# Performance work log

Hardware: AMD Instinct MI355X
Metric: run time of the kernel (lower is better)

Reference implementation:

```python
import jax, jax.numpy as jnp
import numpy as np

N_NODES = 50000
N_EDGES = 800000
IN_DIM = 96
HID = 96
OUT_DIM = 32
N_GRAPHS = 256


def setup_inputs() -> dict:
    key = jax.random.key(0)
    ks = jax.random.split(key, 12)
    x = jax.random.normal(ks[0], (N_NODES, IN_DIM), dtype=jnp.float32)
    edge_index = jax.random.randint(ks[1], (2, N_EDGES), 0, N_NODES, dtype=jnp.int64)
    batch = jnp.sort(jax.random.randint(ks[2], (N_NODES,), 0, N_GRAPHS, dtype=jnp.int64))
    s = 1.0 / np.sqrt(HID)
    W1 = jax.random.normal(ks[3], (IN_DIM, HID), dtype=jnp.float32) * s
    W2 = jax.random.normal(ks[4], (HID, HID), dtype=jnp.float32) * s
    W3 = jax.random.normal(ks[5], (HID, HID), dtype=jnp.float32) * s
    fc_w = jax.random.normal(ks[6], (HID, OUT_DIM), dtype=jnp.float32) * s
    return {
        'x': x, 'edge_index': edge_index, 'batch': batch,
        'W1': W1, 'b1': jnp.zeros((HID,), jnp.float32),
        'W2': W2, 'b2': jnp.zeros((HID,), jnp.float32),
        'W3': W3, 'b3': jnp.zeros((HID,), jnp.float32),
        'fc_w': fc_w, 'fc_b': jnp.zeros((OUT_DIM,), jnp.float32),
    }


def _gcn_conv(h, row, col, norm, W, b, n_nodes):
    # linear transform first (PyG GCNConv), then normalized gather/scatter-add
    h = h @ W                                   # [N, F]
    msg = h[row] * norm[:, None]                # [E+N, F] gather + scale
    out = jax.ops.segment_sum(msg, col, num_segments=n_nodes)
    return out + b


def reference(x, edge_index, batch, W1, b1, W2, b2, W3, b3, fc_w, fc_b):
    n = x.shape[0]
    loop = jnp.arange(n, dtype=edge_index.dtype)
    row = jnp.concatenate([edge_index[0], loop])  # sources (with self-loops)
    col = jnp.concatenate([edge_index[1], loop])  # targets
    # symmetric normalization: deg over targets, norm = d^-1/2[row] * d^-1/2[col]
    deg = jax.ops.segment_sum(jnp.ones_like(col, dtype=x.dtype), col, num_segments=n)
    dis = jnp.where(deg > 0, jax.lax.rsqrt(deg), 0.0)
    norm = dis[row] * dis[col]

    h = jax.nn.relu(_gcn_conv(x, row, col, norm, W1, b1, n))
    h = jax.nn.relu(_gcn_conv(h, row, col, norm, W2, b2, n))
    h = jax.nn.relu(_gcn_conv(h, row, col, norm, W3, b3, n))

    # global_mean_pool over graph ids
    sums = jax.ops.segment_sum(h, batch, num_segments=N_GRAPHS)
    cnts = jax.ops.segment_sum(jnp.ones((n,), h.dtype), batch, num_segments=N_GRAPHS)
    pooled = sums / jnp.maximum(cnts, 1.0)[:, None]
    return pooled @ fc_w + fc_b
```

## Files before the change

kernel.cpp:

```cpp
#include <hip/hip_runtime.h>

#define NN 50000
#define NE 800000
#define F  96
#define F4 24
#define FB 48
#define RB4 12
#define OD 32
#define NG 256
#define CAP 64
#define PROWS 21
#define SHARDS 8
#define SHARD_SZ 6250
#define PERSHARD 64
#define NWF 1152
#define RPB 64
#define TPB 256

typedef unsigned int u32;
typedef unsigned short u16;
typedef short short8 __attribute__((ext_vector_type(8)));
typedef float f32x4 __attribute__((ext_vector_type(4)));

static inline size_t align_up(size_t x) { return (x + 255) & ~(size_t)255; }

__device__ inline u32 f2bf_rne(float x) {
    u32 u = __float_as_uint(x);
    return (u + 0x7fffu + ((u >> 16) & 1u)) >> 16;
}
__device__ inline u32 packbf(float a, float b) {
    return f2bf_rne(a) | (f2bf_rne(b) << 16);
}
__device__ inline float bf_lo(u32 u) { return __uint_as_float(u << 16); }
__device__ inline float bf_hi(u32 u) { return __uint_as_float(u & 0xffff0000u); }

__global__ __launch_bounds__(256) void k_fillb(const int* __restrict__ src,
                                               const int* __restrict__ tgt,
                                               int* __restrict__ cnt,
                                               u16* __restrict__ bucket) {
    int shard = blockIdx.x & (SHARDS - 1);
    int sb    = blockIdx.x >> 3;
    int lo    = shard * SHARD_SZ;
    int hi    = lo + SHARD_SZ;
    const int4* tgt4 = reinterpret_cast<const int4*>(tgt);
    const int4* src4 = reinterpret_cast<const int4*>(src);
    const int nchunk = NE / 4;
    for (int c = sb * 256 + threadIdx.x; c < nchunk; c += PERSHARD * 256) {
        int4 t4 = tgt4[c];
        int4 s4 = src4[c];
        if (t4.x >= lo && t4.x < hi) {
            int p = atomicAdd(&cnt[t4.x], 1);
            if (p < CAP) bucket[t4.x * CAP + p] = (u16)s4.x;
        }
        if (t4.y >= lo && t4.y < hi) {
            int p = atomicAdd(&cnt[t4.y], 1);
            if (p < CAP) bucket[t4.y * CAP + p] = (u16)s4.y;
        }
        if (t4.z >= lo && t4.z < hi) {
            int p = atomicAdd(&cnt[t4.z], 1);
            if (p < CAP) bucket[t4.z * CAP + p] = (u16)s4.z;
        }
        if (t4.w >= lo && t4.w < hi) {
            int p = atomicAdd(&cnt[t4.w], 1);
            if (p < CAP) bucket[t4.w * CAP + p] = (u16)s4.w;
        }
    }
}

__global__ __launch_bounds__(256) void k_dis(const int* __restrict__ cnt, float* __restrict__ dis) {
    int i = blockIdx.x * 256 + threadIdx.x;
    if (i < NN) dis[i] = rsqrtf((float)(cnt[i] + 1));
}

__global__ __launch_bounds__(256) void k_cvt(const float4* __restrict__ x4,
                                             const float* __restrict__ dis,
                                             uint4* __restrict__ rb4) {
    int i = blockIdx.x * 256 + threadIdx.x;
    if (i >= NN * RB4) return;
    int v = i / RB4;
    float dv = dis[v];
    float4 f0 = x4[(size_t)i * 2];
    float4 f1 = x4[(size_t)i * 2 + 1];
    rb4[i] = make_uint4(packbf(dv * f0.x, dv * f0.y), packbf(dv * f0.z, dv * f0.w),
                        packbf(dv * f1.x, dv * f1.y), packbf(dv * f1.z, dv * f1.w));
}

__global__ __launch_bounds__(256) void k_wprep3(const float* __restrict__ W1,
                                                const float* __restrict__ W2,
                                                const float* __restrict__ W3,
                                                uint4* __restrict__ wf) {
    int e = blockIdx.x * 256 + threadIdx.x;
    if (e >= 3 * NWF) return;
    int wi = e / NWF;
    int f  = e - wi * NWF;
    const float* W = (wi == 0) ? W1 : ((wi == 1) ? W2 : W3);
    int n  = f & 15;
    int t1 = f >> 4;
    int quad = t1 & 3;
    int t2 = t1 >> 2;
    int kc = t2 % 3;
    int ct = t2 / 3;
    int k  = kc * 32 + quad * 8;
    int col = ct * 16 + n;
    u32 w0 = packbf(W[(k + 0) * F + col], W[(k + 1) * F + col]);
    u32 w1 = packbf(W[(k + 2) * F + col], W[(k + 3) * F + col]);
    u32 w2 = packbf(W[(k + 4) * F + col], W[(k + 5) * F + col]);
    u32 w3 = packbf(W[(k + 6) * F + col], W[(k + 7) * F + col]);
    wf[e] = make_uint4(w0, w1, w2, w3);
}

__global__ __launch_bounds__(TPB) void k_layer(const uint4* __restrict__ rprev,
                                               const uint4* __restrict__ wfragG,
                                               const int* __restrict__ cnt,
                                               const u16* __restrict__ bucket,
                                               const float* __restrict__ dis,
                                               const float* __restrict__ bias,
                                               const int last,
                                               u16* __restrict__ rnext) {
    __shared__ uint4 atile[RPB * 13];
    int tid = threadIdx.x;
    int r0 = blockIdx.x * RPB;

    const u32* hb = reinterpret_cast<const u32*>(rprev);

#pragma unroll
    for (int it = 0; it < 3; ++it) {
        int slot = it * TPB + tid;
        int ln  = slot / 12;
        int sub = slot - ln * 12;
        int v = r0 + ln;
        uint4 res = make_uint4(0u, 0u, 0u, 0u);
        if (v < NN) {
            int co = sub * 4;
            uint4 hv = *reinterpret_cast<const uint4*>(&hb[(size_t)v * FB + co]);
            float a0 = bf_lo(hv.x), a1 = bf_hi(hv.x);
            float a2 = bf_lo(hv.y), a3 = bf_hi(hv.y);
            float a4 = bf_lo(hv.z), a5 = bf_hi(hv.z);
            float a6 = bf_lo(hv.w), a7 = bf_hi(hv.w);

            int deg = cnt[v];
            if (deg > CAP) deg = CAP;
            const u16* bkt = &bucket[v * CAP];
            int e = 0;
            for (; e + 7 < deg; e += 8) {
                uint4 b8 = *reinterpret_cast<const uint4*>(&bkt[e]);
                int s0 = b8.x & 0xffff, s1 = b8.x >> 16;
                int s2 = b8.y & 0xffff, s3 = b8.y >> 16;
                int s4 = b8.z & 0xffff, s5 = b8.z >> 16;
                int s6 = b8.w & 0xffff, s7 = b8.w >> 16;
                uint4 g0 = *reinterpret_cast<const uint4*>(&hb[(size_t)s0 * FB + co]);
                uint4 g1 = *reinterpret_cast<const uint4*>(&hb[(size_t)s1 * FB + co]);
                uint4 g2 = *reinterpret_cast<const uint4*>(&hb[(size_t)s2 * FB + co]);
                uint4 g3 = *reinterpret_cast<const uint4*>(&hb[(size_t)s3 * FB + co]);
                uint4 g4 = *reinterpret_cast<const uint4*>(&hb[(size_t)s4 * FB + co]);
                uint4 g5 = *reinterpret_cast<const uint4*>(&hb[(size_t)s5 * FB + co]);
                uint4 g6 = *reinterpret_cast<const uint4*>(&hb[(size_t)s6 * FB + co]);
                uint4 g7 = *reinterpret_cast<const uint4*>(&hb[(size_t)s7 * FB + co]);
                a0 += bf_lo(g0.x) + bf_lo(g1.x) + bf_lo(g2.x) + bf_lo(g3.x)
                    + bf_lo(g4.x) + bf_lo(g5.x) + bf_lo(g6.x) + bf_lo(g7.x);
                a1 += bf_hi(g0.x) + bf_hi(g1.x) + bf_hi(g2.x) + bf_hi(g3.x)
                    + bf_hi(g4.x) + bf_hi(g5.x) + bf_hi(g6.x) + bf_hi(g7.x);
                a2 += bf_lo(g0.y) + bf_lo(g1.y) + bf_lo(g2.y) + bf_lo(g3.y)
                    + bf_lo(g4.y) + bf_lo(g5.y) + bf_lo(g6.y) + bf_lo(g7.y);
                a3 += bf_hi(g0.y) + bf_hi(g1.y) + bf_hi(g2.y) + bf_hi(g3.y)
                    + bf_hi(g4.y) + bf_hi(g5.y) + bf_hi(g6.y) + bf_hi(g7.y);
                a4 += bf_lo(g0.z) + bf_lo(g1.z) + bf_lo(g2.z) + bf_lo(g3.z)
                    + bf_lo(g4.z) + bf_lo(g5.z) + bf_lo(g6.z) + bf_lo(g7.z);
                a5 += bf_hi(g0.z) + bf_hi(g1.z) + bf_hi(g2.z) + bf_hi(g3.z)
                    + bf_hi(g4.z) + bf_hi(g5.z) + bf_hi(g6.z) + bf_hi(g7.z);
                a6 += bf_lo(g0.w) + bf_lo(g1.w) + bf_lo(g2.w) + bf_lo(g3.w)
                    + bf_lo(g4.w) + bf_lo(g5.w) + bf_lo(g6.w) + bf_lo(g7.w);
                a7 += bf_hi(g0.w) + bf_hi(g1.w) + bf_hi(g2.w) + bf_hi(g3.w)
                    + bf_hi(g4.w) + bf_hi(g5.w) + bf_hi(g6.w) + bf_hi(g7.w);
            }
            for (; e + 3 < deg; e += 4) {
                uint2 b4 = *reinterpret_cast<const uint2*>(&bkt[e]);
                int s0 = b4.x & 0xffff, s1 = b4.x >> 16;
                int s2 = b4.y & 0xffff, s3 = b4.y >> 16;
                uint4 g0 = *reinterpret_cast<const uint4*>(&hb[(size_t)s0 * FB + co]);
                uint4 g1 = *reinterpret_cast<const uint4*>(&hb[(size_t)s1 * FB + co]);
                uint4 g2 = *reinterpret_cast<const uint4*>(&hb[(size_t)s2 * FB + co]);
                uint4 g3 = *reinterpret_cast<const uint4*>(&hb[(size_t)s3 * FB + co]);
                a0 += bf_lo(g0.x) + bf_lo(g1.x) + bf_lo(g2.x) + bf_lo(g3.x);
                a1 += bf_hi(g0.x) + bf_hi(g1.x) + bf_hi(g2.x) + bf_hi(g3.x);
                a2 += bf_lo(g0.y) + bf_lo(g1.y) + bf_lo(g2.y) + bf_lo(g3.y);
                a3 += bf_hi(g0.y) + bf_hi(g1.y) + bf_hi(g2.y) + bf_hi(g3.y);
                a4 += bf_lo(g0.z) + bf_lo(g1.z) + bf_lo(g2.z) + bf_lo(g3.z);
                a5 += bf_hi(g0.z) + bf_hi(g1.z) + bf_hi(g2.z) + bf_hi(g3.z);
                a6 += bf_lo(g0.w) + bf_lo(g1.w) + bf_lo(g2.w) + bf_lo(g3.w);
                a7 += bf_hi(g0.w) + bf_hi(g1.w) + bf_hi(g2.w) + bf_hi(g3.w);
            }
            for (; e < deg; ++e) {
                int s = bkt[e];
                uint4 g = *reinterpret_cast<const uint4*>(&hb[(size_t)s * FB + co]);
                a0 += bf_lo(g.x); a1 += bf_hi(g.x);
                a2 += bf_lo(g.y); a3 += bf_hi(g.y);
                a4 += bf_lo(g.z); a5 += bf_hi(g.z);
                a6 += bf_lo(g.w); a7 += bf_hi(g.w);
            }
            float dv = dis[v];
            res = make_uint4(packbf(dv * a0, dv * a1), packbf(dv * a2, dv * a3),
                             packbf(dv * a4, dv * a5), packbf(dv * a6, dv * a7));
        }
        atile[ln * 13 + sub] = res;
    }
    __syncthreads();

    int wave = tid >> 6;
    int lane = tid & 63;
    int m    = lane & 15;
    int quad = lane >> 4;
    int arow = wave * 16 + m;

    short8 a0 = *reinterpret_cast<const short8*>(&atile[arow * 13 + 0 * 4 + quad]);
    short8 a1 = *reinterpret_cast<const short8*>(&atile[arow * 13 + 1 * 4 + quad]);
    short8 a2 = *reinterpret_cast<const short8*>(&atile[arow * 13 + 2 * 4 + quad]);

    f32x4 acc[6];
#pragma unroll
    for (int ct = 0; ct < 6; ++ct) acc[ct] = (f32x4)(0.0f);
#pragma unroll
    for (int ct = 0; ct < 6; ++ct) {
        short8 b0 = *reinterpret_cast<const short8*>(&wfragG[((ct * 3 + 0) * 4 + quad) * 16 + m]);
        short8 b1 = *reinterpret_cast<const short8*>(&wfragG[((ct * 3 + 1) * 4 + quad) * 16 + m]);
        short8 b2 = *reinterpret_cast<const short8*>(&wfragG[((ct * 3 + 2) * 4 + quad) * 16 + m]);
        acc[ct] = __builtin_amdgcn_mfma_f32_16x16x32_bf16(a0, b0, acc[ct], 0, 0, 0);
        acc[ct] = __builtin_amdgcn_mfma_f32_16x16x32_bf16(a1, b1, acc[ct], 0, 0, 0);
        acc[ct] = __builtin_amdgcn_mfma_f32_16x16x32_bf16(a2, b2, acc[ct], 0, 0, 0);
    }

    int rbase = r0 + wave * 16 + quad * 4;
    float dr[4];
#pragma unroll
    for (int r = 0; r < 4; ++r) {
        int row = rbase + r;
        dr[r] = (row < NN) ? (last ? 1.0f : dis[row]) : 0.0f;
    }
#pragma unroll
    for (int ct = 0; ct < 6; ++ct) {
        float bb = bias[ct * 16 + m];
#pragma unroll
        for (int r = 0; r < 4; ++r) {
            int row = rbase + r;
            if (row < NN) {
                float h = fmaxf(acc[ct][r] + bb, 0.0f);
                rnext[(size_t)row * F + ct * 16 + m] = (u16)f2bf_rne(h * dr[r]);
            }
        }
    }
}

__device__ inline int lower_bound_i(const int* __restrict__ a, int n, int key) {
    int lo = 0, hi = n;
    while (lo < hi) {
        int mid = (lo + hi) >> 1;
        if (a[mid] < key) lo = mid + 1; else hi = mid;
    }
    return lo;
}

__global__ __launch_bounds__(512) void k_pool(const uint2* __restrict__ hb2,
                                              const int* __restrict__ batch,
                                              float4* __restrict__ pooled4) {
    __shared__ int range[2];
    __shared__ float4 part[PROWS][F4];
    int g = blockIdx.x;
    int t = threadIdx.x;
    if (t == 0) range[0] = lower_bound_i(batch, NN, g);
    if (t == 1) range[1] = lower_bound_i(batch, NN, g + 1);
    __syncthreads();
    int lo = range[0], hi = range[1];
    int row = t / F4;
    int sub = t - row * F4;
    if (row < PROWS) {
        float4 acc = make_float4(0.f, 0.f, 0.f, 0.f);
        for (int v = lo + row; v < hi; v += PROWS) {
            uint2 xv = hb2[(size_t)v * F4 + sub];
            acc.x += bf_lo(xv.x); acc.y += bf_hi(xv.x);
            acc.z += bf_lo(xv.y); acc.w += bf_hi(xv.y);
        }
        part[row][sub] = acc;
    }
    __syncthreads();
    if (t < F4) {
        float4 s = part[0][t];
        for (int r = 1; r < PROWS; ++r) {
            float4 p = part[r][t];
            s.x += p.x; s.y += p.y; s.z += p.z; s.w += p.w;
        }
        float inv = 1.0f / fmaxf((float)(hi - lo), 1.0f);
        s.x *= inv; s.y *= inv; s.z *= inv; s.w *= inv;
        pooled4[g * F4 + t] = s;
    }
}

__global__ __launch_bounds__(256) void k_fc(const float* __restrict__ pooled,
                                            const float* __restrict__ fcw,
                                            const float* __restrict__ fcb,
                                            float* __restrict__ out) {
    int i = blockIdx.x * 256 + threadIdx.x;
    if (i >= NG * OD) return;
    int g = i >> 5;
    int o = i & 31;
    float acc = 0.0f;
    for (int f = 0; f < F; ++f) acc += pooled[g * F + f] * fcw[f * OD + o];
    out[i] = acc + fcb[o];
}

extern "C" void kernel_launch(void* const* d_in, const int* in_sizes, int n_in,
                              void* d_out, int out_size, void* d_ws, size_t ws_size,
                              hipStream_t stream) {
    (void)in_sizes; (void)n_in; (void)out_size; (void)ws_size;
    const float* x    = (const float*)d_in[0];
    const int*   ei   = (const int*)d_in[1];
    const int*   batc = (const int*)d_in[2];
    const float* W1   = (const float*)d_in[3];
    const float* b1   = (const float*)d_in[4];
    const float* W2   = (const float*)d_in[5];
    const float* b2   = (const float*)d_in[6];
    const float* W3   = (const float*)d_in[7];
    const float* b3   = (const float*)d_in[8];
    const float* fcw  = (const float*)d_in[9];
    const float* fcb  = (const float*)d_in[10];
    float* out = (float*)d_out;

    const int* src = ei;
    const int* tgt = ei + NE;

    char* ws = (char*)d_ws;
    int*    cnt    = (int*)ws;    ws += align_up((size_t)NN * 4);
    float*  dis    = (float*)ws;  ws += align_up((size_t)NN * 4);
    u16*    bucket = (u16*)ws;    ws += align_up((size_t)NN * CAP * 2);
    u32*    rA     = (u32*)ws;    ws += align_up((size_t)NN * FB * 4);
    u32*    rB     = (u32*)ws;    ws += align_up((size_t)NN * FB * 4);
    uint4*  wfrag3 = (uint4*)ws;  ws += align_up((size_t)3 * NWF * 16);
    float*  pooled = (float*)ws;  ws += align_up((size_t)NG * F * 4);

    const int B = 256;
    const int node_grid  = (NN + B - 1) / B;
    const int cvt_grid   = (NN * RB4 + B - 1) / B;
    const int wprep_grid = (3 * NWF + B - 1) / B;
    const int layer_grid = (NN + RPB - 1) / RPB;

    (void)hipMemsetAsync(cnt, 0, (size_t)NN * 4, stream);
    k_fillb <<<SHARDS * PERSHARD, B, 0, stream>>>(src, tgt, cnt, bucket);
    k_dis   <<<node_grid, B, 0, stream>>>(cnt, dis);
    k_wprep3<<<wprep_grid, B, 0, stream>>>(W1, W2, W3, wfrag3);
    k_cvt   <<<cvt_grid, B, 0, stream>>>((const float4*)x, dis, (uint4*)rA);

    k_layer<<<layer_grid, TPB, 0, stream>>>((const uint4*)rA, wfrag3 + 0 * NWF,
                                            cnt, bucket, dis, b1, 0, (u16*)rB);
    k_layer<<<layer_grid, TPB, 0, stream>>>((const uint4*)rB, wfrag3 + 1 * NWF,
                                            cnt, bucket, dis, b2, 0, (u16*)rA);
    k_layer<<<layer_grid, TPB, 0, stream>>>((const uint4*)rA, wfrag3 + 2 * NWF,
                                            cnt, bucket, dis, b3, 1, (u16*)rB);

    k_pool<<<NG, 512, 0, stream>>>((const uint2*)rB, batc, (float4*)pooled);
    k_fc  <<<(NG * OD + B - 1) / B, B, 0, stream>>>(pooled, fcw, fcb, out);
}
```

Measured before the change: 245.8 us.

## Sort nodes by degree for balanced layer work and pack edge pairs

Adds a counting sort of nodes by in-degree (histogram, scan, permutation kernels), and the layer kernel processes nodes in that permuted order so rows handled by one wave have similar gather lengths, which reduces divergence. Also packs source/target into one 32-bit word per edge before bucket filling, so that kernel reads half as much. The cost is four extra small launches, including a single-thread scan. Permuted processing also makes output writes scattered and node-feature reads less local.

New measurement: 381.3 us. 55.1% more time.

```diff
diff --git a/kernel.cpp b/kernel.cpp
--- a/kernel.cpp
+++ b/kernel.cpp
@@ -3,7 +3,6 @@
 #define NN 50000
 #define NE 800000
 #define F  96
-#define F4 24
 #define FB 48
 #define RB4 12
 #define OD 32
@@ -16,6 +15,7 @@
 #define NWF 1152
 #define RPB 64
 #define TPB 256
+#define NBINS 65
 
 typedef unsigned int u32;
 typedef unsigned short u16;
@@ -34,35 +34,46 @@
 __device__ inline float bf_lo(u32 u) { return __uint_as_float(u << 16); }
 __device__ inline float bf_hi(u32 u) { return __uint_as_float(u & 0xffff0000u); }
 
-__global__ __launch_bounds__(256) void k_fillb(const int* __restrict__ src,
-                                               const int* __restrict__ tgt,
+__global__ __launch_bounds__(256) void k_pack(const int* __restrict__ src,
+                                              const int* __restrict__ tgt,
+                                              uint4* __restrict__ ep4) {
+    int c = blockIdx.x * 256 + threadIdx.x;
+    if (c >= NE / 4) return;
+    int4 s4 = reinterpret_cast<const int4*>(src)[c];
+    int4 t4 = reinterpret_cast<const int4*>(tgt)[c];
+    ep4[c] = make_uint4(((u32)t4.x << 16) | (u32)s4.x, ((u32)t4.y << 16) | (u32)s4.y,
+                        ((u32)t4.z << 16) | (u32)s4.z, ((u32)t4.w << 16) | (u32)s4.w);
+}
+
+__global__ __launch_bounds__(256) void k_fillb(const uint4* __restrict__ ep4,
                                                int* __restrict__ cnt,
                                                u16* __restrict__ bucket) {
     int shard = blockIdx.x & (SHARDS - 1);
     int sb    = blockIdx.x >> 3;
     int lo    = shard * SHARD_SZ;
     int hi    = lo + SHARD_SZ;
-    const int4* tgt4 = reinterpret_cast<const int4*>(tgt);
-    const int4* src4 = reinterpret_cast<const int4*>(src);
     const int nchunk = NE / 4;
     for (int c = sb * 256 + threadIdx.x; c < nchunk; c += PERSHARD * 256) {
-        int4 t4 = tgt4[c];
-        int4 s4 = src4[c];
-        if (t4.x >= lo && t4.x < hi) {
-            int p = atomicAdd(&cnt[t4.x], 1);
-            if (p < CAP) bucket[t4.x * CAP + p] = (u16)s4.x;
-        }
-        if (t4.y >= lo && t4.y < hi) {
-            int p = atomicAdd(&cnt[t4.y], 1);
-            if (p < CAP) bucket[t4.y * CAP + p] = (u16)s4.y;
-        }
-        if (t4.z >= lo && t4.z < hi) {
-            int p = atomicAdd(&cnt[t4.z], 1);
-            if (p < CAP) bucket[t4.z * CAP + p] = (u16)s4.z;
-        }
-        if (t4.w >= lo && t4.w < hi) {
-            int p = atomicAdd(&cnt[t4.w], 1);
-            if (p < CAP) bucket[t4.w * CAP + p] = (u16)s4.w;
+        uint4 p = ep4[c];
+        int t0 = p.x >> 16, s0 = p.x & 0xffff;
+        int t1 = p.y >> 16, s1 = p.y & 0xffff;
+        int t2 = p.z >> 16, s2 = p.z & 0xffff;
+        int t3 = p.w >> 16, s3 = p.w & 0xffff;
+        if (t0 >= lo && t0 < hi) {
+            int q = atomicAdd(&cnt[t0], 1);
+            if (q < CAP) bucket[t0 * CAP + q] = (u16)s0;
+        }
+        if (t1 >= lo && t1 < hi) {
+            int q = atomicAdd(&cnt[t1], 1);
+            if (q < CAP) bucket[t1 * CAP + q] = (u16)s1;
+        }
+        if (t2 >= lo && t2 < hi) {
+            int q = atomicAdd(&cnt[t2], 1);
+            if (q < CAP) bucket[t2 * CAP + q] = (u16)s2;
+        }
+        if (t3 >= lo && t3 < hi) {
+            int q = atomicAdd(&cnt[t3], 1);
+            if (q < CAP) bucket[t3 * CAP + q] = (u16)s3;
         }
     }
 }
@@ -70,6 +81,38 @@
 __global__ __launch_bounds__(256) void k_dis(const int* __restrict__ cnt, float* __restrict__ dis) {
     int i = blockIdx.x * 256 + threadIdx.x;
     if (i < NN) dis[i] = rsqrtf((float)(cnt[i] + 1));
+}
+
+__global__ __launch_bounds__(256) void k_hist(const int* __restrict__ cnt, int* __restrict__ hist) {
+    __shared__ int h[NBINS];
+    int t = threadIdx.x;
+    if (t < NBINS) h[t] = 0;
+    __syncthreads();
+    int i = blockIdx.x * 256 + t;
+    if (i < NN) {
+        int d = cnt[i]; if (d > CAP) d = CAP;
+        atomicAdd(&h[d], 1);
+    }
+    __syncthreads();
+    if (t < NBINS && h[t]) atomicAdd(&hist[t], h[t]);
+}
+
+__global__ void k_scan(const int* __restrict__ hist, int* __restrict__ base) {
+    if (threadIdx.x == 0) {
+        int s = 0;
+        for (int d = 0; d < NBINS; ++d) { base[d] = s; s += hist[d]; }
+    }
+}
+
+__global__ __launch_bounds__(256) void k_perm(const int* __restrict__ cnt,
+                                              int* __restrict__ base,
+                                              int* __restrict__ perm) {
+    int i = blockIdx.x * 256 + threadIdx.x;
+    if (i < NN) {
+        int d = cnt[i]; if (d > CAP) d = CAP;
+        int pos = atomicAdd(&base[d], 1);
+        perm[pos] = i;
+    }
 }
 
 __global__ __launch_bounds__(256) void k_cvt(const float4* __restrict__ x4,
@@ -115,6 +158,7 @@
                                                const u16* __restrict__ bucket,
                                                const float* __restrict__ dis,
                                                const float* __restrict__ bias,
+                                               const int* __restrict__ perm,
                                                const int last,
                                                u16* __restrict__ rnext) {
     __shared__ uint4 atile[RPB * 13];
@@ -128,9 +172,9 @@
         int slot = it * TPB + tid;
         int ln  = slot / 12;
         int sub = slot - ln * 12;
-        int v = r0 + ln;
         uint4 res = make_uint4(0u, 0u, 0u, 0u);
-        if (v < NN) {
+        if (r0 + ln < NN) {
+            int v = perm[r0 + ln];
             int co = sub * 4;
             uint4 hv = *reinterpret_cast<const uint4*>(&hb[(size_t)v * FB + co]);
             float a0 = bf_lo(hv.x), a1 = bf_hi(hv.x);
@@ -230,21 +274,27 @@
     }
 
     int rbase = r0 + wave * 16 + quad * 4;
+    int orow[4];
     float dr[4];
 #pragma unroll
     for (int r = 0; r < 4; ++r) {
         int row = rbase + r;
-        dr[r] = (row < NN) ? (last ? 1.0f : dis[row]) : 0.0f;
+        if (row < NN) {
+            orow[r] = perm[row];
+            dr[r]   = last ? 1.0f : dis[orow[r]];
+        } else {
+            orow[r] = -1;
+            dr[r]   = 0.0f;
+        }
     }
 #pragma unroll
     for (int ct = 0; ct < 6; ++ct) {
         float bb = bias[ct * 16 + m];
 #pragma unroll
         for (int r = 0; r < 4; ++r) {
-            int row = rbase + r;
-            if (row < NN) {
+            if (orow[r] >= 0) {
                 float h = fmaxf(acc[ct][r] + bb, 0.0f);
-                rnext[(size_t)row * F + ct * 16 + m] = (u16)f2bf_rne(h * dr[r]);
+                rnext[(size_t)orow[r] * F + ct * 16 + m] = (u16)f2bf_rne(h * dr[r]);
             }
         }
     }
@@ -263,26 +313,26 @@
                                               const int* __restrict__ batch,
                                               float4* __restrict__ pooled4) {
     __shared__ int range[2];
-    __shared__ float4 part[PROWS][F4];
+    __shared__ float4 part[PROWS][24];
     int g = blockIdx.x;
     int t = threadIdx.x;
     if (t == 0) range[0] = lower_bound_i(batch, NN, g);
     if (t == 1) range[1] = lower_bound_i(batch, NN, g + 1);
     __syncthreads();
     int lo = range[0], hi = range[1];
-    int row = t / F4;
-    int sub = t - row * F4;
+    int row = t / 24;
+    int sub = t - row * 24;
     if (row < PROWS) {
         float4 acc = make_float4(0.f, 0.f, 0.f, 0.f);
         for (int v = lo + row; v < hi; v += PROWS) {
-            uint2 xv = hb2[(size_t)v * F4 + sub];
+            uint2 xv = hb2[(size_t)v * 24 + sub];
             acc.x += bf_lo(xv.x); acc.y += bf_hi(xv.x);
             acc.z += bf_lo(xv.y); acc.w += bf_hi(xv.y);
         }
         part[row][sub] = acc;
     }
     __syncthreads();
-    if (t < F4) {
+    if (t < 24) {
         float4 s = part[0][t];
         for (int r = 1; r < PROWS; ++r) {
             float4 p = part[r][t];
@@ -290,7 +340,7 @@
         }
         float inv = 1.0f / fmaxf((float)(hi - lo), 1.0f);
         s.x *= inv; s.y *= inv; s.z *= inv; s.w *= inv;
-        pooled4[g * F4 + t] = s;
+        pooled4[g * 24 + t] = s;
     }
 }
 
@@ -328,9 +378,13 @@
     const int* tgt = ei + NE;
 
     char* ws = (char*)d_ws;
-    int*    cnt    = (int*)ws;    ws += align_up((size_t)NN * 4);
+    int*    cnt    = (int*)ws;    ws += align_up((size_t)(NN + 2 * NBINS) * 4);
+    int*    hist   = cnt + NN;
+    int*    base   = hist + NBINS;
     float*  dis    = (float*)ws;  ws += align_up((size_t)NN * 4);
+    int*    perm   = (int*)ws;    ws += align_up((size_t)NN * 4);
     u16*    bucket = (u16*)ws;    ws += align_up((size_t)NN * CAP * 2);
+    u32*    ep     = (u32*)ws;    ws += align_up((size_t)NE * 4);
     u32*    rA     = (u32*)ws;    ws += align_up((size_t)NN * FB * 4);
     u32*    rB     = (u32*)ws;    ws += align_up((size_t)NN * FB * 4);
     uint4*  wfrag3 = (uint4*)ws;  ws += align_up((size_t)3 * NWF * 16);
@@ -340,20 +394,25 @@
     const int node_grid  = (NN + B - 1) / B;
     const int cvt_grid   = (NN * RB4 + B - 1) / B;
     const int wprep_grid = (3 * NWF + B - 1) / B;
+    const int pack_grid  = (NE / 4 + B - 1) / B;
     const int layer_grid = (NN + RPB - 1) / RPB;
 
-    (void)hipMemsetAsync(cnt, 0, (size_t)NN * 4, stream);
-    k_fillb <<<SHARDS * PERSHARD, B, 0, stream>>>(src, tgt, cnt, bucket);
+    (void)hipMemsetAsync(cnt, 0, (size_t)(NN + 2 * NBINS) * 4, stream);
+    k_pack  <<<pack_grid, B, 0, stream>>>(src, tgt, (uint4*)ep);
+    k_fillb <<<SHARDS * PERSHARD, B, 0, stream>>>((const uint4*)ep, cnt, bucket);
     k_dis   <<<node_grid, B, 0, stream>>>(cnt, dis);
+    k_hist  <<<node_grid, B, 0, stream>>>(cnt, hist);
+    k_scan  <<<1, 64, 0, stream>>>(hist, base);
+    k_perm  <<<node_grid, B, 0, stream>>>(cnt, base, perm);
     k_wprep3<<<wprep_grid, B, 0, stream>>>(W1, W2, W3, wfrag3);
     k_cvt   <<<cvt_grid, B, 0, stream>>>((const float4*)x, dis, (uint4*)rA);
 
     k_layer<<<layer_grid, TPB, 0, stream>>>((const uint4*)rA, wfrag3 + 0 * NWF,
-                                            cnt, bucket, dis, b1, 0, (u16*)rB);
+                                            cnt, bucket, dis, b1, perm, 0, (u16*)rB);
     k_layer<<<layer_grid, TPB, 0, stream>>>((const uint4*)rB, wfrag3 + 1 * NWF,
-                                            cnt, bucket, dis, b2, 0, (u16*)rA);
+                                            cnt, bucket, dis, b2, perm, 0, (u16*)rA);
     k_layer<<<layer_grid, TPB, 0, stream>>>((const uint4*)rA, wfrag3 + 2 * NWF,
-                                            cnt, bucket, dis, b3, 1, (u16*)rB);
+                                            cnt, bucket, dis, b3, perm, 1, (u16*)rB);
 
     k_pool<<<NG, 512, 0, stream>>>((const uint2*)rB, batc, (float4*)pooled);
     k_fc  <<<(NG * OD + B - 1) / B, B, 0, stream>>>(pooled, fcw, fcb, out);
```
